# Performance work log

Measured on AMD Instinct MI355X. Metric: run time of the kernel, lower is better.

Reference implementation:

```python
import jax, jax.numpy as jnp
import numpy as np

VOCAB = 1000
MAX_T = 1000  # max_episode_length
L = 64        # instruction length


def _uniform(key, shape, fan_in, fan_out):
    bound = float(np.sqrt(6.0 / (fan_in + fan_out)))
    return jax.random.uniform(key, shape, jnp.float32, -bound, bound)


def setup_inputs() -> dict:
    key = jax.random.key(0)
    ks = jax.random.split(key, 20)
    s = float(1.0 / np.sqrt(256.0))
    inp = {}
    inp['x'] = jax.random.normal(ks[0], (1, 400), jnp.float32)
    inp['input_inst'] = jax.random.randint(ks[1], (1, L), 0, VOCAB)
    inp['tx'] = jax.random.randint(ks[2], (1,), 0, MAX_T + 1)
    inp['hx'] = jax.random.normal(ks[3], (1, 256), jnp.float32) * 0.1
    inp['cx'] = jax.random.normal(ks[4], (1, 256), jnp.float32) * 0.1
    inp['img1_w'] = _uniform(ks[5], (128, 400), 400, 128); inp['img1_b'] = jnp.zeros((128,), jnp.float32)
    inp['img2_w'] = _uniform(ks[6], (128, 128), 128, 128); inp['img2_b'] = jnp.zeros((128,), jnp.float32)
    inp['img3_w'] = _uniform(ks[7], (128, 128), 128, 128); inp['img3_b'] = jnp.zeros((128,), jnp.float32)
    inp['emb'] = jax.random.normal(ks[8], (VOCAB, 32), jnp.float32)
    inp['gru_wi'] = jax.random.uniform(ks[9], (768, 32), jnp.float32, -s, s)
    inp['gru_wh'] = jax.random.uniform(ks[10], (768, 256), jnp.float32, -s, s)
    inp['gru_bi'] = jnp.zeros((768,), jnp.float32); inp['gru_bh'] = jnp.zeros((768,), jnp.float32)
    inp['attn_w'] = _uniform(ks[11], (128, 256), 256, 128); inp['attn_b'] = jnp.zeros((128,), jnp.float32)
    inp['time_emb'] = jax.random.normal(ks[12], (MAX_T + 1, 32), jnp.float32)
    inp['lin_w'] = _uniform(ks[13], (256, 128), 128, 256); inp['lin_b'] = jnp.zeros((256,), jnp.float32)
    inp['lstm_wi'] = jax.random.uniform(ks[14], (1024, 256), jnp.float32, -s, s)
    inp['lstm_wh'] = jax.random.uniform(ks[15], (1024, 256), jnp.float32, -s, s)
    inp['lstm_bi'] = jnp.zeros((1024,), jnp.float32); inp['lstm_bh'] = jnp.zeros((1024,), jnp.float32)
    inp['crit_w'] = jax.random.normal(ks[16], (1, 288), jnp.float32) * 0.06
    inp['crit_b'] = jnp.zeros((1,), jnp.float32)
    inp['act_w'] = jax.random.normal(ks[17], (4, 288), jnp.float32) * 0.01
    inp['act_b'] = jnp.zeros((4,), jnp.float32)
    return inp


def _linear(x, w, b):
    return x @ w.T + b


def reference(x, input_inst, tx, hx, cx,
              img1_w, img1_b, img2_w, img2_b, img3_w, img3_b,
              emb, gru_wi, gru_wh, gru_bi, gru_bh,
              attn_w, attn_b, time_emb, lin_w, lin_b,
              lstm_wi, lstm_wh, lstm_bi, lstm_bh,
              crit_w, crit_b, act_w, act_b):
    # image MLP: 400 -> 128 -> 128 -> 128
    h = jax.nn.relu(_linear(x.reshape(x.shape[0], -1), img1_w, img1_b))
    h = jax.nn.relu(_linear(h, img2_w, img2_b))
    x_image_rep = jax.nn.relu(_linear(h, img3_w, img3_b))  # (1,128)

    # GRU encoder over instruction tokens (torch gate order: r, z, n)
    emb_seq = emb[input_inst[0]]  # (L, 32)

    def gru_step(hg, e):
        gi = gru_wi @ e + gru_bi        # (768,)
        gh = gru_wh @ hg + gru_bh       # (768,)
        ir, iz, i_n = jnp.split(gi, 3)
        hr, hz, hn = jnp.split(gh, 3)
        r = jax.nn.sigmoid(ir + hr)
        z = jax.nn.sigmoid(iz + hz)
        n = jnp.tanh(i_n + r * hn)
        return (1.0 - z) * n + z * hg, None

    h_enc, _ = jax.lax.scan(gru_step, jnp.zeros((256,), x.dtype), emb_seq)
    x_instr_rep = h_enc[None, :]  # (1,256)

    # gated attention fusion
    x_attention = jax.nn.sigmoid(_linear(x_instr_rep, attn_w, attn_b))  # (1,128)
    fused = x_image_rep * x_attention
    fused = jax.nn.relu(_linear(fused, lin_w, lin_b))  # (1,256)

    # LSTMCell (torch gate order: i, f, g, o)
    gates = fused @ lstm_wi.T + lstm_bi + hx @ lstm_wh.T + lstm_bh  # (1,1024)
    i_g, f_g, g_g, o_g = jnp.split(gates, 4, axis=1)
    c_new = jax.nn.sigmoid(f_g) * cx + jax.nn.sigmoid(i_g) * jnp.tanh(g_g)
    h_new = jax.nn.sigmoid(o_g) * jnp.tanh(c_new)

    t_emb = time_emb[tx].reshape(-1, 32)  # (1,32)
    feat = jnp.concatenate([h_new, t_emb], axis=1)  # (1,288)
    return _linear(feat, crit_w, crit_b), _linear(feat, act_w, act_b), h_new, c_new
```

## Files before the change

### kernel.cpp

```cpp
#include <hip/hip_runtime.h>
#include <math.h>


typedef __fp16 h2 __attribute__((ext_vector_type(2)));
typedef __fp16 h4 __attribute__((ext_vector_type(4)));
typedef __fp16 h8 __attribute__((ext_vector_type(8)));
typedef float  f4v __attribute__((ext_vector_type(4)));

#define WS_IMG    0
#define WS_GATESH 128
#define WS_FUSED  1152

__device__ __forceinline__ float dot4(const float4 a, const float4 b){
  return a.x*b.x + a.y*b.y + a.z*b.z + a.w*b.w;
}
__device__ __forceinline__ float sigm(float x){ return 1.f/(1.f+expf(-x)); }

#define P0(v) __builtin_shufflevector(v,v,0,1)
#define P1(v) __builtin_shufflevector(v,v,2,3)
#define P2(v) __builtin_shufflevector(v,v,4,5)
#define P3(v) __builtin_shufflevector(v,v,6,7)
#define PK(a,b) __builtin_amdgcn_cvt_pkrtz(a,b)
#define FD(w,e,acc) __builtin_amdgcn_fdot2(w,e,acc,false)

__device__ __forceinline__ h8 pack8(const float4 a, const float4 b){
  const h2 p0=PK(a.x,a.y), p1=PK(a.z,a.w), p2=PK(b.x,b.y), p3=PK(b.z,b.w);
  const h4 q0=__builtin_shufflevector(p0,p1,0,1,2,3);
  const h4 q1=__builtin_shufflevector(p2,p3,0,1,2,3);
  return __builtin_shufflevector(q0,q1,0,1,2,3,4,5,6,7);
}

__global__ __launch_bounds__(256) void a3c_pre(
    const float* __restrict__ x,
    const float* __restrict__ i1w, const float* __restrict__ i1b,
    const float* __restrict__ i2w, const float* __restrict__ i2b,
    const float* __restrict__ i3w, const float* __restrict__ i3b,
    const float* __restrict__ hx,  const float* __restrict__ lwh,
    const float* __restrict__ lbh,
    const int*   __restrict__ tx,  const float* __restrict__ temb,
    const float* __restrict__ cw,  const float* __restrict__ cb,
    const float* __restrict__ acw, const float* __restrict__ acb,
    float* __restrict__ ws, float* __restrict__ out)
{
  const int b = blockIdx.x;
  const int t = threadIdx.x;

  if (b == 0) {
    __shared__ __align__(16) float x_lds[400];
    __shared__ __align__(16) float h1[128];
    __shared__ __align__(16) float h2s[128];
    x_lds[t] = x[t];
    if (t < 144) x_lds[256+t] = x[256+t];
    __syncthreads();
    {
      const int o = t>>1, half = t&1;
      const float4* wr = (const float4*)(i1w + o*400 + half*200);
      const float4* xr = (const float4*)(x_lds + half*200);
      float acc = 0.f;
      #pragma unroll 5
      for (int k=0;k<50;++k) acc += dot4(wr[k], xr[k]);
      acc += __shfl_down(acc, 1, 2);
      if (half == 0) h1[o] = fmaxf(acc + i1b[o], 0.f);
    }
    __syncthreads();
    if (t < 128){
      const float4* wr = (const float4*)(i2w + t*128);
      const float4* h4p = (const float4*)h1;
      float acc = i2b[t];
      #pragma unroll 8
      for (int k=0;k<32;++k) acc += dot4(wr[k], h4p[k]);
      h2s[t] = fmaxf(acc, 0.f);
    }
    __syncthreads();
    if (t < 128){
      const float4* wr = (const float4*)(i3w + t*128);
      const float4* h4p = (const float4*)h2s;
      float acc = i3b[t];
      #pragma unroll 8
      for (int k=0;k<32;++k) acc += dot4(wr[k], h4p[k]);
      ws[WS_IMG + t] = fmaxf(acc, 0.f);
    }

  } else if (b == 5) {
    if (t < 64){
      float tv = 0.f;
      if (t < 32) tv = temb[tx[0]*32 + t];
      #pragma unroll
      for (int o=0;o<5;++o){
        const float* wrow = (o==0) ? cw : (acw + (o-1)*288);
        float pr = (t < 32) ? tv*wrow[256+t] : 0.f;
        #pragma unroll
        for (int off=16; off; off>>=1) pr += __shfl_down(pr, off, 32);
        if (t == 0) out[o] = pr + ((o==0) ? cb[0] : acb[o-1]);
      }
    }

  } else {
    __shared__ __align__(16) float hx_lds[256];
    hx_lds[t] = hx[t];
    __syncthreads();
    const int R = (b-1)*256 + t;
    const float4* wr = (const float4*)(lwh + R*256);
    const float4* h4p = (const float4*)hx_lds;
    float acc = lbh[R];
    #pragma unroll 8
    for (int k=0;k<64;++k) acc += dot4(wr[k], h4p[k]);
    ws[WS_GATESH + R] = acc;
  }
}

__global__ __launch_bounds__(768) __attribute__((amdgpu_waves_per_eu(3, 3)))
void a3c_scan(
    const int*   __restrict__ inst, const float* __restrict__ emb,
    const float* __restrict__ gwi,  const float* __restrict__ gwh,
    const float* __restrict__ gbi,  const float* __restrict__ gbh,
    const float* __restrict__ aw,   const float* __restrict__ ab,
    const float* __restrict__ lw,   const float* __restrict__ lb,
    float* __restrict__ ws)
{
  const int t    = threadIdx.x;
  const int lane = t & 63;
  const int wv   = t >> 6;
  const int arow = lane & 15;
  const int kgrp = lane >> 4;
  const int koff = kgrp * 8;
  const int rows0 = wv * 64;

  __shared__ __fp16 gi16[64*768];
  __shared__ __align__(16) __fp16 e16[2048];
  __shared__ __align__(16) __fp16 h16[256];
  __shared__ float h32[256];
  __shared__ __align__(16) float acc_lds[768];
  __shared__ float bh_lds[768];
  __shared__ __align__(16) float f0[128];

  for (int i=t; i<2048; i+=768)
    e16[i] = (__fp16)emb[inst[i>>5]*32 + (i&31)];
  bh_lds[t] = gbh[t];
  const float bi_t = gbi[t];
  __syncthreads();

  {
    const float4* wp = (const float4*)(gwi + t*32);
    const float4 qa=wp[0], qb=wp[1], qc=wp[2], qd=wp[3],
                 qe=wp[4], qf=wp[5], qg=wp[6], qh=wp[7];
    const h2 wi0=PK(qa.x,qa.y), wi1=PK(qa.z,qa.w), wi2=PK(qb.x,qb.y), wi3=PK(qb.z,qb.w);
    const h2 wi4=PK(qc.x,qc.y), wi5=PK(qc.z,qc.w), wi6=PK(qd.x,qd.y), wi7=PK(qd.z,qd.w);
    const h2 wi8=PK(qe.x,qe.y), wi9=PK(qe.z,qe.w), wiA=PK(qf.x,qf.y), wiB=PK(qf.z,qf.w);
    const h2 wiC=PK(qg.x,qg.y), wiD=PK(qg.z,qg.w), wiE=PK(qh.x,qh.y), wiF=PK(qh.z,qh.w);
    for (int s=0;s<64;++s){
      const h8* ech = (const h8*)(e16 + s*32);
      const h8 e0=ech[0], e1=ech[1], e2=ech[2], e3=ech[3];
      float g = bi_t;
      g=FD(wi0,P0(e0),g); g=FD(wi1,P1(e0),g); g=FD(wi2,P2(e0),g); g=FD(wi3,P3(e0),g);
      g=FD(wi4,P0(e1),g); g=FD(wi5,P1(e1),g); g=FD(wi6,P2(e1),g); g=FD(wi7,P3(e1),g);
      g=FD(wi8,P0(e2),g); g=FD(wi9,P1(e2),g); g=FD(wiA,P2(e2),g); g=FD(wiB,P3(e2),g);
      g=FD(wiC,P0(e3),g); g=FD(wiD,P1(e3),g); g=FD(wiE,P2(e3),g); g=FD(wiF,P3(e3),g);
      gi16[s*768 + t] = (__fp16)g;
    }
  }

  h8 F0_0,F0_1,F0_2,F0_3,F0_4,F0_5,F0_6,F0_7;
  h8 F1_0,F1_1,F1_2,F1_3,F1_4,F1_5,F1_6,F1_7;
  h8 F2_0,F2_1,F2_2,F2_3,F2_4,F2_5,F2_6,F2_7;
  h8 F3_0,F3_1,F3_2,F3_3,F3_4,F3_5,F3_6,F3_7;
  #define LOADF(T,K) { \
    const float4* wp = (const float4*)(gwh + (rows0 + (T)*16 + arow)*256 + (K)*32 + koff); \
    F##T##_##K = pack8(wp[0], wp[1]); }
  LOADF(0,0) LOADF(0,1) LOADF(0,2) LOADF(0,3) LOADF(0,4) LOADF(0,5) LOADF(0,6) LOADF(0,7)
  LOADF(1,0) LOADF(1,1) LOADF(1,2) LOADF(1,3) LOADF(1,4) LOADF(1,5) LOADF(1,6) LOADF(1,7)
  LOADF(2,0) LOADF(2,1) LOADF(2,2) LOADF(2,3) LOADF(2,4) LOADF(2,5) LOADF(2,6) LOADF(2,7)
  LOADF(3,0) LOADF(3,1) LOADF(3,2) LOADF(3,3) LOADF(3,4) LOADF(3,5) LOADF(3,6) LOADF(3,7)
  #undef LOADF

  if (t < 256){ h32[t] = 0.f; h16[t] = (__fp16)0.f; }
  __syncthreads();

  const h8 hzero = {0,0,0,0,0,0,0,0};
  for (int s=0;s<64;++s){
    const h8 hv = *(const h8*)(h16 + koff);
    const h8 bf = (arow == 0) ? hv : hzero;
    f4v d0={0.f,0.f,0.f,0.f}, d1={0.f,0.f,0.f,0.f},
        d2={0.f,0.f,0.f,0.f}, d3={0.f,0.f,0.f,0.f};
    #define MMK(K) \
      d0 = __builtin_amdgcn_mfma_f32_16x16x32_f16(F0_##K, bf, d0, 0,0,0); \
      d1 = __builtin_amdgcn_mfma_f32_16x16x32_f16(F1_##K, bf, d1, 0,0,0); \
      d2 = __builtin_amdgcn_mfma_f32_16x16x32_f16(F2_##K, bf, d2, 0,0,0); \
      d3 = __builtin_amdgcn_mfma_f32_16x16x32_f16(F3_##K, bf, d3, 0,0,0);
    MMK(0) MMK(1) MMK(2) MMK(3) MMK(4) MMK(5) MMK(6) MMK(7)
    #undef MMK
    if (arow == 0){
      const int rb = kgrp*4;
      *(f4v*)(acc_lds + rows0      + rb) = d0;
      *(f4v*)(acc_lds + rows0 + 16 + rb) = d1;
      *(f4v*)(acc_lds + rows0 + 32 + rb) = d2;
      *(f4v*)(acc_lds + rows0 + 48 + rb) = d3;
    }
    __syncthreads();
    if (t < 256){
      const float ar = acc_lds[t]       + bh_lds[t];
      const float az = acc_lds[256 + t] + bh_lds[256 + t];
      const float an = acc_lds[512 + t] + bh_lds[512 + t];
      const float r  = sigm((float)gi16[s*768 + t]       + ar);
      const float z  = sigm((float)gi16[s*768 + 256 + t] + az);
      const float n  = tanhf((float)gi16[s*768 + 512 + t] + r*an);
      const float hvv = (1.f - z)*n + z*h32[t];
      h32[t] = hvv;
      h16[t] = (__fp16)hvv;
    }
    __syncthreads();
  }

  if (t < 128){
    const float4* wr = (const float4*)(aw + t*256);
    const float4* h4p = (const float4*)h32;
    float acc = ab[t];
    #pragma unroll 8
    for (int k=0;k<64;++k) acc += dot4(wr[k], h4p[k]);
    f0[t] = ws[WS_IMG + t] * sigm(acc);
  }
  __syncthreads();
  if (t < 256){
    const float4* wr = (const float4*)(lw + t*128);
    const float4* h4p = (const float4*)f0;
    float acc = lb[t];
    #pragma unroll 8
    for (int k=0;k<32;++k) acc += dot4(wr[k], h4p[k]);
    ws[WS_FUSED + t] = fmaxf(acc, 0.f);
  }
}

__global__ __launch_bounds__(256) void a3c_post(
    const float* __restrict__ lwi, const float* __restrict__ lbi,
    const float* __restrict__ cx,
    const float* __restrict__ cw,  const float* __restrict__ acw,
    float* __restrict__ ws, float* __restrict__ out)
{
  const int p = blockIdx.x;
  const int t = threadIdx.x;
  __shared__ __align__(16) float fused_lds[256];
  __shared__ float gv[256];
  __shared__ float hh[64];
  fused_lds[t] = ws[WS_FUSED + t];
  __syncthreads();
  const int g = t>>6, ul = t&63;
  const int R = (g<<8) + p*64 + ul;
  const float4* wr = (const float4*)(lwi + R*256);
  const float4* f4p = (const float4*)fused_lds;
  float acc = ws[WS_GATESH + R] + lbi[R];
  #pragma unroll 8
  for (int k=0;k<64;++k) acc += dot4(wr[k], f4p[k]);
  gv[t] = acc;
  __syncthreads();
  if (t < 64){
    const int u2 = p*64 + t;
    const float iv = gv[t], fv = gv[64+t], gg = gv[128+t], ov = gv[192+t];
    const float c = sigm(fv)*cx[u2] + sigm(iv)*tanhf(gg);
    const float h = sigm(ov)*tanhf(c);
    out[5   + u2] = h;
    out[261 + u2] = c;
    hh[t] = h;
  }
  __syncthreads();
  if (t < 64){
    #pragma unroll
    for (int o=0;o<5;++o){
      const float* wrow = (o==0) ? cw : (acw + (o-1)*288);
      float pr = hh[t]*wrow[p*64 + t];
      #pragma unroll
      for (int off=32; off; off>>=1) pr += __shfl_down(pr, off, 64);
      if (t == 0) atomicAdd(out + o, pr);
    }
  }
}

extern "C" void kernel_launch(void* const* d_in, const int* in_sizes, int n_in,
                              void* d_out, int out_size, void* d_ws, size_t ws_size,
                              hipStream_t stream) {
  (void)in_sizes; (void)n_in; (void)out_size; (void)ws_size;
  const float* x    = (const float*)d_in[0];
  const int*   inst = (const int*)  d_in[1];
  const int*   tx   = (const int*)  d_in[2];
  const float* hx   = (const float*)d_in[3];
  const float* cx   = (const float*)d_in[4];
  const float* i1w  = (const float*)d_in[5];
  const float* i1b  = (const float*)d_in[6];
  const float* i2w  = (const float*)d_in[7];
  const float* i2b  = (const float*)d_in[8];
  const float* i3w  = (const float*)d_in[9];
  const float* i3b  = (const float*)d_in[10];
  const float* emb  = (const float*)d_in[11];
  const float* gwi  = (const float*)d_in[12];
  const float* gwh  = (const float*)d_in[13];
  const float* gbi  = (const float*)d_in[14];
  const float* gbh  = (const float*)d_in[15];
  const float* aw   = (const float*)d_in[16];
  const float* ab   = (const float*)d_in[17];
  const float* temb = (const float*)d_in[18];
  const float* lw   = (const float*)d_in[19];
  const float* lb   = (const float*)d_in[20];
  const float* lwi  = (const float*)d_in[21];
  const float* lwh  = (const float*)d_in[22];
  const float* lbi  = (const float*)d_in[23];
  const float* lbh  = (const float*)d_in[24];
  const float* cw   = (const float*)d_in[25];
  const float* cb   = (const float*)d_in[26];
  const float* acw  = (const float*)d_in[27];
  const float* acb  = (const float*)d_in[28];
  float* ws  = (float*)d_ws;
  float* out = (float*)d_out;

  a3c_pre <<<6, 256, 0, stream>>>(x, i1w, i1b, i2w, i2b, i3w, i3b,
                                  hx, lwh, lbh, tx, temb, cw, cb, acw, acb,
                                  ws, out);
  a3c_scan<<<1, 768, 0, stream>>>(inst, emb, gwi, gwh, gbi, gbh,
                                  aw, ab, lw, lb, ws);
  a3c_post<<<4, 256, 0, stream>>>(lwi, lbi, cx, cw, acw, ws, out);
}
```

Before: 146.5 us.

## Replace MFMA GRU recurrence matvec with register-resident fdot2 paired-row dot products

The recurrent GRU matvec drops the MFMA path, which wasted 15 of 16 columns on a single vector and needed an LDS round trip for the accumulators. Each thread now keeps two rows' half-slices of the recurrent weights in registers as fp16 and computes them with fdot2. Partial sums are combined across the thread pair with a shuffle. The thread also folds in the input-gate value and bias before writing gate pre-activations to LDS, and a VGPR budget is pinned to fit 168 registers. This trades matrix-core throughput for lower per-step latency, with a risk of register pressure or spills.

```diff
diff --git a/kernel.cpp b/kernel.cpp
--- a/kernel.cpp
+++ b/kernel.cpp
@@ -5,7 +5,6 @@
 typedef __fp16 h2 __attribute__((ext_vector_type(2)));
 typedef __fp16 h4 __attribute__((ext_vector_type(4)));
 typedef __fp16 h8 __attribute__((ext_vector_type(8)));
-typedef float  f4v __attribute__((ext_vector_type(4)));
 
 #define WS_IMG    0
 #define WS_GATESH 128
@@ -109,7 +108,8 @@
   }
 }
 
-__global__ __launch_bounds__(768) __attribute__((amdgpu_waves_per_eu(3, 3)))
+__global__ __launch_bounds__(768)
+__attribute__((amdgpu_waves_per_eu(3, 3), amdgpu_num_vgpr(168)))
 void a3c_scan(
     const int*   __restrict__ inst, const float* __restrict__ emb,
     const float* __restrict__ gwi,  const float* __restrict__ gwh,
@@ -118,25 +118,20 @@
     const float* __restrict__ lw,   const float* __restrict__ lb,
     float* __restrict__ ws)
 {
-  const int t    = threadIdx.x;
-  const int lane = t & 63;
-  const int wv   = t >> 6;
-  const int arow = lane & 15;
-  const int kgrp = lane >> 4;
-  const int koff = kgrp * 8;
-  const int rows0 = wv * 64;
-
+  const int t = threadIdx.x;
+  const int p = t >> 1;
+  const int j = t & 1;
   __shared__ __fp16 gi16[64*768];
   __shared__ __align__(16) __fp16 e16[2048];
+  __shared__ __align__(16) float h32[256];
   __shared__ __align__(16) __fp16 h16[256];
-  __shared__ float h32[256];
-  __shared__ __align__(16) float acc_lds[768];
-  __shared__ float bh_lds[768];
+  __shared__ float pre[768];
+  __shared__ float hn[256];
   __shared__ __align__(16) float f0[128];
 
   for (int i=t; i<2048; i+=768)
     e16[i] = (__fp16)emb[inst[i>>5]*32 + (i&31)];
-  bh_lds[t] = gbh[t];
+  const float bh_t = gbh[t];
   const float bi_t = gbi[t];
   __syncthreads();
 
@@ -160,53 +155,52 @@
     }
   }
 
-  h8 F0_0,F0_1,F0_2,F0_3,F0_4,F0_5,F0_6,F0_7;
-  h8 F1_0,F1_1,F1_2,F1_3,F1_4,F1_5,F1_6,F1_7;
-  h8 F2_0,F2_1,F2_2,F2_3,F2_4,F2_5,F2_6,F2_7;
-  h8 F3_0,F3_1,F3_2,F3_3,F3_4,F3_5,F3_6,F3_7;
-  #define LOADF(T,K) { \
-    const float4* wp = (const float4*)(gwh + (rows0 + (T)*16 + arow)*256 + (K)*32 + koff); \
-    F##T##_##K = pack8(wp[0], wp[1]); }
-  LOADF(0,0) LOADF(0,1) LOADF(0,2) LOADF(0,3) LOADF(0,4) LOADF(0,5) LOADF(0,6) LOADF(0,7)
-  LOADF(1,0) LOADF(1,1) LOADF(1,2) LOADF(1,3) LOADF(1,4) LOADF(1,5) LOADF(1,6) LOADF(1,7)
-  LOADF(2,0) LOADF(2,1) LOADF(2,2) LOADF(2,3) LOADF(2,4) LOADF(2,5) LOADF(2,6) LOADF(2,7)
-  LOADF(3,0) LOADF(3,1) LOADF(3,2) LOADF(3,3) LOADF(3,4) LOADF(3,5) LOADF(3,6) LOADF(3,7)
-  #undef LOADF
-
+  h8 wA0,wA1,wA2,wA3,wA4,wA5,wA6,wA7,wA8,wA9,wAa,wAb,wAc,wAd,wAe,wAf;
+  h8 wB0,wB1,wB2,wB3,wB4,wB5,wB6,wB7,wB8,wB9,wBa,wBb,wBc,wBd,wBe,wBf;
+  {
+    const float4* wp0 = (const float4*)(gwh + (2*p  )*256 + 128*j);
+    const float4* wp1 = (const float4*)(gwh + (2*p+1)*256 + 128*j);
+    #define LW(dst, base, c) dst = pack8((base)[2*(c)], (base)[2*(c)+1]);
+    LW(wA0,wp0,0)  LW(wA1,wp0,1)  LW(wA2,wp0,2)  LW(wA3,wp0,3)
+    LW(wA4,wp0,4)  LW(wA5,wp0,5)  LW(wA6,wp0,6)  LW(wA7,wp0,7)
+    LW(wA8,wp0,8)  LW(wA9,wp0,9)  LW(wAa,wp0,10) LW(wAb,wp0,11)
+    LW(wAc,wp0,12) LW(wAd,wp0,13) LW(wAe,wp0,14) LW(wAf,wp0,15)
+    LW(wB0,wp1,0)  LW(wB1,wp1,1)  LW(wB2,wp1,2)  LW(wB3,wp1,3)
+    LW(wB4,wp1,4)  LW(wB5,wp1,5)  LW(wB6,wp1,6)  LW(wB7,wp1,7)
+    LW(wB8,wp1,8)  LW(wB9,wp1,9)  LW(wBa,wp1,10) LW(wBb,wp1,11)
+    LW(wBc,wp1,12) LW(wBd,wp1,13) LW(wBe,wp1,14) LW(wBf,wp1,15)
+    #undef LW
+  }
   if (t < 256){ h32[t] = 0.f; h16[t] = (__fp16)0.f; }
   __syncthreads();
 
-  const h8 hzero = {0,0,0,0,0,0,0,0};
+  const h8* hch = (const h8*)(h16 + 128*j);
   for (int s=0;s<64;++s){
-    const h8 hv = *(const h8*)(h16 + koff);
-    const h8 bf = (arow == 0) ? hv : hzero;
-    f4v d0={0.f,0.f,0.f,0.f}, d1={0.f,0.f,0.f,0.f},
-        d2={0.f,0.f,0.f,0.f}, d3={0.f,0.f,0.f,0.f};
-    #define MMK(K) \
-      d0 = __builtin_amdgcn_mfma_f32_16x16x32_f16(F0_##K, bf, d0, 0,0,0); \
-      d1 = __builtin_amdgcn_mfma_f32_16x16x32_f16(F1_##K, bf, d1, 0,0,0); \
-      d2 = __builtin_amdgcn_mfma_f32_16x16x32_f16(F2_##K, bf, d2, 0,0,0); \
-      d3 = __builtin_amdgcn_mfma_f32_16x16x32_f16(F3_##K, bf, d3, 0,0,0);
-    MMK(0) MMK(1) MMK(2) MMK(3) MMK(4) MMK(5) MMK(6) MMK(7)
-    #undef MMK
-    if (arow == 0){
-      const int rb = kgrp*4;
-      *(f4v*)(acc_lds + rows0      + rb) = d0;
-      *(f4v*)(acc_lds + rows0 + 16 + rb) = d1;
-      *(f4v*)(acc_lds + rows0 + 32 + rb) = d2;
-      *(f4v*)(acc_lds + rows0 + 48 + rb) = d3;
-    }
+    const float gi_s = (float)gi16[s*768 + t];
+    float a0 = 0.f, a1 = 0.f;
+    #define DOTC(c, W0, W1) { const h8 hv = hch[c]; \
+      a0=FD(P0(W0),P0(hv),a0); a1=FD(P0(W1),P0(hv),a1); \
+      a0=FD(P1(W0),P1(hv),a0); a1=FD(P1(W1),P1(hv),a1); \
+      a0=FD(P2(W0),P2(hv),a0); a1=FD(P2(W1),P2(hv),a1); \
+      a0=FD(P3(W0),P3(hv),a0); a1=FD(P3(W1),P3(hv),a1); }
+    DOTC(0,wA0,wB0)   DOTC(1,wA1,wB1)   DOTC(2,wA2,wB2)   DOTC(3,wA3,wB3)
+    DOTC(4,wA4,wB4)   DOTC(5,wA5,wB5)   DOTC(6,wA6,wB6)   DOTC(7,wA7,wB7)
+    DOTC(8,wA8,wB8)   DOTC(9,wA9,wB9)   DOTC(10,wAa,wBa)  DOTC(11,wAb,wBb)
+    DOTC(12,wAc,wBc)  DOTC(13,wAd,wBd)  DOTC(14,wAe,wBe)  DOTC(15,wAf,wBf)
+    #undef DOTC
+    const float keep = j ? a1 : a0;
+    const float send = j ? a0 : a1;
+    const float acc  = keep + __shfl_xor(send, 1) + bh_t;
+    if (t < 512) pre[t] = gi_s + acc;
+    else       { pre[t] = gi_s; hn[t-512] = acc; }
     __syncthreads();
     if (t < 256){
-      const float ar = acc_lds[t]       + bh_lds[t];
-      const float az = acc_lds[256 + t] + bh_lds[256 + t];
-      const float an = acc_lds[512 + t] + bh_lds[512 + t];
-      const float r  = sigm((float)gi16[s*768 + t]       + ar);
-      const float z  = sigm((float)gi16[s*768 + 256 + t] + az);
-      const float n  = tanhf((float)gi16[s*768 + 512 + t] + r*an);
-      const float hvv = (1.f - z)*n + z*h32[t];
-      h32[t] = hvv;
-      h16[t] = (__fp16)hvv;
+      const float r  = sigm(pre[t]);
+      const float z  = sigm(pre[256+t]);
+      const float n  = tanhf(pre[512+t] + r*hn[t]);
+      const float hv = (1.f - z)*n + z*h32[t];
+      h32[t] = hv;
+      h16[t] = (__fp16)hv;
     }
     __syncthreads();
   }
```

Result: slower. 158.3 us (+8.1%).
